# Optimization experiments

Hardware: AMD Instinct MI355X
Metric: run time of the kernel (lower is better)

## Reference

```python
import jax, jax.numpy as jnp
import numpy as np

H, B, F, D1, D21, D22, C = 10, 16384, 4, 2048, 2048, 2048, 2
OBS_X, OBS_Y, RADIUS = 40.0, 15.0, 6.0


def setup_inputs() -> dict:
    key = jax.random.key(0)
    ks = jax.random.split(key, 12)
    s = 0.02  # weight scale
    return {
        'x':   jax.random.normal(ks[0], (B, F), jnp.float32),
        'W1':  jax.random.normal(ks[1], (H, F, D1), jnp.float32) * s,
        'b1':  jnp.zeros((H, D1), jnp.float32),
        'W21': jax.random.normal(ks[2], (H, D1, D21), jnp.float32) * s,
        'b21': jnp.zeros((H, D21), jnp.float32),
        'W22': jax.random.normal(ks[3], (H, D1, D22), jnp.float32) * s,
        'b22': jnp.zeros((H, D22), jnp.float32),
        'W31': jax.random.normal(ks[4], (H, D21, C), jnp.float32) * s,
        'b31': jnp.zeros((H, C), jnp.float32),
        'W32': jax.random.normal(ks[5], (H, D22, C), jnp.float32) * s,
        'b32': jnp.zeros((H, C), jnp.float32),
        'wt':  jnp.ones((H,), jnp.float32),
        'mean': jax.random.normal(ks[6], (F,), jnp.float32),
        'std':  jnp.ones((F,), jnp.float32),
        'sgn': 1,
        'itr': 0,
    }


def reference(x, W1, b1, W21, b21, W22, b22, W31, b31, W32, b32, wt, mean, std, sgn, itr):
    # x: [B,F]; un-normalized state x0 = x*std + mean
    x0 = x * std + mean

    # --- 10-head small-MLP ensemble (batched over heads via einsum) ---
    h1  = jax.nn.relu(jnp.einsum('bf,hfd->hbd', x, W1) + b1[:, None, :])      # [H,B,D1]
    x21 = jax.nn.relu(jnp.einsum('hbd,hde->hbe', h1, W21) + b21[:, None, :])  # [H,B,D21]
    x22 = jax.nn.relu(jnp.einsum('hbd,hde->hbe', h1, W22) + b22[:, None, :])  # [H,B,D22]
    x31 = jnp.einsum('hbe,hec->hbc', x21, W31) + b31[:, None, :]              # [H,B,C] nominal control
    x32 = 4.0 * jax.nn.sigmoid(jnp.einsum('hbe,hec->hbc', x22, W32) + b32[:, None, :])  # [H,B,C] CBF params

    # --- dCBF constraint (shared across heads; depends only on x0) ---
    px, py, theta, v = x0[:, 0], x0[:, 1], x0[:, 2], x0[:, 3]
    dx, dy = px - OBS_X, py - OBS_Y
    st, ct = jnp.sin(theta), jnp.cos(theta)
    barrier = dx * dx + dy * dy - RADIUS * RADIUS                 # [B]
    barrier_dot = 2.0 * dx * v * ct + 2.0 * dy * v * st          # [B]
    Lf2b = 2.0 * v * v                                            # [B]
    LgLfbu1 = -2.0 * dx * v * st + 2.0 * dy * v * ct
    LgLfbu2 = 2.0 * dx * ct + 2.0 * dy * st
    G = jnp.stack([-LgLfbu1, -LgLfbu2], axis=-1)                  # [B,C]

    # sgn == 1 -> same branch for every head (i==0 or sgn==1)
    h_rhs = Lf2b + (x32[..., 0] + x32[..., 1]) * barrier_dot + x32[..., 0] * x32[..., 1] * barrier  # [H,B]

    # --- batched QP: min 0.5 u'u - x31'u  s.t. G u <= h  (Q = I) ---
    # closed-form single-constraint active set: u = x31 - relu(G.x31 - h)/||G||^2 * G
    Gu = jnp.einsum('bc,hbc->hb', G, x31)                         # [H,B]
    GG = jnp.sum(G * G, axis=-1)                                  # [B]
    lam = jax.nn.relu(Gu - h_rhs) / GG                            # [H,B]
    u = x31 - lam[..., None] * G[None, :, :]                      # [H,B,C]

    # --- softmax-weighted ensemble sum ---
    w = jax.nn.softmax(wt)                                        # [H]
    return jnp.einsum('h,hbc->bc', w, u)                          # [B,C]
```

## Files before the change

### kernel.cpp

```cpp
#include <hip/hip_runtime.h>
#include <hip/hip_bf16.h>
#include <stdint.h>

#define H_  10
#define B_  16384
#define F_  4
#define D_  2048
#define C_  2

typedef __attribute__((ext_vector_type(8)))  short  short8;
typedef __attribute__((ext_vector_type(16))) float  floatx16;

typedef const uint32_t __attribute__((address_space(1))) gu32;
typedef uint32_t       __attribute__((address_space(3))) lu32;

__device__ __forceinline__ void async16(const void* g, void* l) {
    __builtin_amdgcn_global_load_lds((gu32*)g, (lu32*)l, 16, 0, 0);
}

__device__ __forceinline__ short8 bc8(uint4 v) { return __builtin_bit_cast(short8, v); }

__device__ __forceinline__ uint32_t packbf(float a, float b) {
    a = fmaxf(a, 0.f); b = fmaxf(b, 0.f);
    const uint32_t ax = __builtin_bit_cast(uint32_t, a) + 0x8000u;
    const uint32_t bx = __builtin_bit_cast(uint32_t, b) + 0x8000u;
    return (ax >> 16) | (bx & 0xFFFF0000u);
}

__device__ __forceinline__ uint32_t f2bf(float f) {
    union { float f; uint32_t u; } a; a.f = f;
    uint32_t u = a.u;
    u += 0x7FFF + ((u >> 16) & 1);
    return u >> 16;
}
__device__ __forceinline__ uint32_t pack2bf(float a, float b) {
    return f2bf(a) | (f2bf(b) << 16);
}


__global__ __launch_bounds__(256) void k_convert(
    const float* __restrict__ W21, const float* __restrict__ W22,
    uint16_t* __restrict__ Bc)
{
    __shared__ float tile[64][65];
    const int z = blockIdx.z;
    const int h = z % H_;
    const float* src = (z < H_ ? W21 : W22) + (size_t)h * D_ * D_;
    uint16_t*   dst  = Bc + (size_t)h * 2 * D_ * D_ + (z < H_ ? 0 : (size_t)D_ * D_);
    const int k0 = blockIdx.x * 64, n0 = blockIdx.y * 64;
    const int t = threadIdx.x;

    const int c4 = (t & 15) * 4;
    const int rb = (t >> 4) * 4;
#pragma unroll
    for (int i = 0; i < 4; i++) {
        const float4 v = *(const float4*)(src + (size_t)(k0 + rb + i) * D_ + n0 + c4);
        tile[rb + i][c4 + 0] = v.x; tile[rb + i][c4 + 1] = v.y;
        tile[rb + i][c4 + 2] = v.z; tile[rb + i][c4 + 3] = v.w;
    }
    __syncthreads();
    const int n = t >> 2;
    const int cb = (t & 3) * 2;
#pragma unroll
    for (int j = 0; j < 2; j++) {
        const int kk = (cb + j) * 8;
        uint32_t pk[4];
#pragma unroll
        for (int e = 0; e < 4; e++)
            pk[e] = pack2bf(tile[kk + 2 * e][n], tile[kk + 2 * e + 1][n]);
        *(uint4*)(dst + (size_t)(n0 + n) * D_ + k0 + kk) = make_uint4(pk[0], pk[1], pk[2], pk[3]);
    }
}

__global__ __launch_bounds__(256) void k_zero(uint4* p, int n4) {
    const int i = blockIdx.x * 256 + threadIdx.x;
    if (i < n4) p[i] = make_uint4(0u, 0u, 0u, 0u);
}

__global__ __launch_bounds__(256) void k_h1(
    const float* __restrict__ x, const float* __restrict__ W1,
    const float* __restrict__ b1, uint16_t* __restrict__ h1t, int h)
{
    const int t = threadIdx.x;
    const int kc = t & 127;
    const int rh = t >> 7;
    const int k0 = kc * 16;
    const float* W1h = W1 + (size_t)h * F_ * D_;
    float w[4][16], bb[16];
#pragma unroll
    for (int f = 0; f < 4; f++)
#pragma unroll
        for (int j = 0; j < 16; j += 4) {
            const float4 v = *(const float4*)(W1h + f * D_ + k0 + j);
            w[f][j] = v.x; w[f][j+1] = v.y; w[f][j+2] = v.z; w[f][j+3] = v.w;
        }
#pragma unroll
    for (int j = 0; j < 16; j += 4) {
        const float4 v = *(const float4*)(b1 + (size_t)h * D_ + k0 + j);
        bb[j] = v.x; bb[j+1] = v.y; bb[j+2] = v.z; bb[j+3] = v.w;
    }
    const int rowBase = blockIdx.x * 16 + rh * 8;
#pragma unroll
    for (int rr = 0; rr < 8; rr++) {
        const int row = rowBase + rr;
        const float4 xv = *(const float4*)(x + (size_t)row * 4);
        uint32_t pk[8];
#pragma unroll
        for (int j = 0; j < 16; j += 2) {
            float aa = fmaf(xv.x, w[0][j], bb[j]);
            aa = fmaf(xv.y, w[1][j], aa);
            aa = fmaf(xv.z, w[2][j], aa);
            aa = fmaf(xv.w, w[3][j], aa);
            float bv = fmaf(xv.x, w[0][j+1], bb[j+1]);
            bv = fmaf(xv.y, w[1][j+1], bv);
            bv = fmaf(xv.z, w[2][j+1], bv);
            bv = fmaf(xv.w, w[3][j+1], bv);
            pk[j >> 1] = packbf(aa, bv);
        }
        uint16_t* d = h1t + (size_t)row * D_ + k0;
        *(uint4*)d       = make_uint4(pk[0], pk[1], pk[2], pk[3]);
        *(uint4*)(d + 8) = make_uint4(pk[4], pk[5], pk[6], pk[7]);
    }
}

__global__ __launch_bounds__(256, 2) void k_gemm(
    const uint16_t* __restrict__ h1t, const uint16_t* __restrict__ Bcw,
    const float* __restrict__ b21, const float* __restrict__ b22,
    const float* __restrict__ W31, const float* __restrict__ W32,
    float* __restrict__ acc31, float* __restrict__ acc32, int h)
{
    __shared__ uint4 smem[3072];

    const int bid = blockIdx.x;
    const int xcd = bid & 7, idx = bid >> 3;
    const int mt = xcd * 16 + (idx & 15), nt = idx >> 4;
    const int mBase = mt * 128, nBase = nt * 256;

    const int t = threadIdx.x;
    const int lane = t & 63, wid = t >> 6;
    const int l31 = lane & 31, hi = lane >> 5;

    const int srow   = lane >> 3;
    const int schunk = (lane & 7) ^ srow;

    const uint16_t* Ag = h1t + (size_t)(mBase + wid * 8 + srow) * D_ + schunk * 8;
    const uint16_t* Bg = Bcw + (size_t)h * (4096 * (size_t)D_)
                             + (size_t)(nBase + wid * 8 + srow) * D_ + schunk * 8;

    floatx16 acc[4][2];
#pragma unroll
    for (int mi = 0; mi < 4; mi++)
#pragma unroll
        for (int nj = 0; nj < 2; nj++)
#pragma unroll
            for (int e = 0; e < 16; e++) acc[mi][nj][e] = 0.f;

    const int x7 = l31 & 7;

    for (int kt = 0; kt < D_; kt += 64) {
#pragma unroll
        for (int i = 0; i < 4; i++)
            async16(Ag + (size_t)(i * 32) * D_ + kt, smem + i * 256 + wid * 64);
#pragma unroll
        for (int i = 0; i < 8; i++)
            async16(Bg + (size_t)(i * 32) * D_ + kt, smem + 1024 + i * 256 + wid * 64);
        asm volatile("s_waitcnt vmcnt(0)" ::: "memory");
        __builtin_amdgcn_sched_barrier(0);
        __builtin_amdgcn_s_barrier();

        __builtin_amdgcn_s_setprio(1);
#pragma unroll
        for (int kk = 0; kk < 4; kk++) {
            const int cx = (kk * 2 + hi) ^ x7;
            short8 af[4], bf[2];
#pragma unroll
            for (int mi = 0; mi < 4; mi++)
                af[mi] = bc8(smem[(mi * 32 + l31) * 8 + cx]);
#pragma unroll
            for (int nj = 0; nj < 2; nj++)
                bf[nj] = bc8(smem[1024 + (wid * 64 + nj * 32 + l31) * 8 + cx]);
#pragma unroll
            for (int mi = 0; mi < 4; mi++)
#pragma unroll
                for (int nj = 0; nj < 2; nj++)
                    acc[mi][nj] = __builtin_amdgcn_mfma_f32_32x32x16_bf16(
                        af[mi], bf[nj], acc[mi][nj], 0, 0, 0);
        }
        __builtin_amdgcn_s_setprio(0);
        __syncthreads();
    }

    const int p    = nBase >> 11;
    const int nloc = nBase & 2047;
    const float* b2p = (p ? b22 : b21) + (size_t)h * D_;
    const float* W3p = (p ? W32 : W31) + (size_t)h * D_ * C_;
    float* ab = (p ? acc32 : acc31) + (size_t)h * B_ * C_;

    float bs[2], w3x[2], w3y[2];
#pragma unroll
    for (int nj = 0; nj < 2; nj++) {
        const int e = nloc + wid * 64 + nj * 32 + l31;
        bs[nj] = b2p[e];
        const float2 w2 = *(const float2*)(W3p + e * 2);
        w3x[nj] = w2.x; w3y[nj] = w2.y;
    }
#pragma unroll
    for (int mi = 0; mi < 4; mi++)
#pragma unroll
        for (int r = 0; r < 16; r++) {
            const float v0 = fmaxf(acc[mi][0][r] + bs[0], 0.f);
            const float v1 = fmaxf(acc[mi][1][r] + bs[1], 0.f);
            float s0 = fmaf(v0, w3x[0], v1 * w3x[1]);
            float s1 = fmaf(v0, w3y[0], v1 * w3y[1]);
#pragma unroll
            for (int off = 1; off < 32; off <<= 1) {
                s0 += __shfl_xor(s0, off, 64);
                s1 += __shfl_xor(s1, off, 64);
            }
            if (l31 == 0) {
                const int row = mBase + mi * 32 + (r & 3) + 8 * (r >> 2) + 4 * hi;
                atomicAdd(&ab[row * C_ + 0], s0);
                atomicAdd(&ab[row * C_ + 1], s1);
            }
        }
}

__global__ __launch_bounds__(256) void k_final(
    const float* __restrict__ x,
    const float* __restrict__ acc31, const float* __restrict__ acc32,
    const float* __restrict__ b31, const float* __restrict__ b32,
    const float* __restrict__ wt, const float* __restrict__ mean,
    const float* __restrict__ stdv, float* __restrict__ out)
{
    const int b = blockIdx.x * 256 + threadIdx.x;
    const float4 xb = *(const float4*)(x + (size_t)b * 4);
    const float px = xb.x * stdv[0] + mean[0];
    const float py = xb.y * stdv[1] + mean[1];
    const float th = xb.z * stdv[2] + mean[2];
    const float v  = xb.w * stdv[3] + mean[3];
    const float dx = px - 40.0f, dy = py - 15.0f;
    const float st = sinf(th), ct = cosf(th);
    const float barrier = dx * dx + dy * dy - 36.0f;
    const float bdot = 2.f * dx * v * ct + 2.f * dy * v * st;
    const float Lf2b = 2.f * v * v;
    const float G0 = -(-2.f * dx * v * st + 2.f * dy * v * ct);
    const float G1 = -(2.f * dx * ct + 2.f * dy * st);
    const float GG = G0 * G0 + G1 * G1;

    float we[H_];
    float wmax = wt[0];
    for (int h = 1; h < H_; h++) wmax = fmaxf(wmax, wt[h]);
    float wsum = 0.f;
    for (int h = 0; h < H_; h++) { we[h] = expf(wt[h] - wmax); wsum += we[h]; }

    float o0 = 0.f, o1 = 0.f;
#pragma unroll
    for (int h = 0; h < H_; h++) {
        const size_t idx = ((size_t)h * B_ + b) * 2;
        const float x310 = acc31[idx]     + b31[h * 2];
        const float x311 = acc31[idx + 1] + b31[h * 2 + 1];
        const float z0 = acc32[idx]     + b32[h * 2];
        const float z1 = acc32[idx + 1] + b32[h * 2 + 1];
        const float x320 = 4.f / (1.f + expf(-z0));
        const float x321 = 4.f / (1.f + expf(-z1));
        const float hr = Lf2b + (x320 + x321) * bdot + x320 * x321 * barrier;
        const float Gu = G0 * x310 + G1 * x311;
        const float lam = fmaxf(Gu - hr, 0.f) / GG;
        o0 += we[h] * (x310 - lam * G0);
        o1 += we[h] * (x311 - lam * G1);
    }
    out[b * 2]     = o0 / wsum;
    out[b * 2 + 1] = o1 / wsum;
}

extern "C" void kernel_launch(void* const* d_in, const int* in_sizes, int n_in,
                              void* d_out, int out_size, void* d_ws, size_t ws_size,
                              hipStream_t stream)
{
    const float* x    = (const float*)d_in[0];
    const float* W1   = (const float*)d_in[1];
    const float* b1   = (const float*)d_in[2];
    const float* W21  = (const float*)d_in[3];
    const float* b21  = (const float*)d_in[4];
    const float* W22  = (const float*)d_in[5];
    const float* b22  = (const float*)d_in[6];
    const float* W31  = (const float*)d_in[7];
    const float* b31  = (const float*)d_in[8];
    const float* W32  = (const float*)d_in[9];
    const float* b32  = (const float*)d_in[10];
    const float* wt   = (const float*)d_in[11];
    const float* mean = (const float*)d_in[12];
    const float* stdv = (const float*)d_in[13];
    float* out = (float*)d_out;

    char* ws = (char*)d_ws;
    uint16_t* Bc   = (uint16_t*)(ws);
    float* acc31   = (float*)(ws + 167772160);
    float* acc32   = (float*)(ws + 169082880);
    uint16_t* h1t  = (uint16_t*)(ws + 170393600);

    k_convert<<<dim3(32, 32, 20), 256, 0, stream>>>(W21, W22, Bc);
    k_zero<<<dim3(640), 256, 0, stream>>>((uint4*)acc31, 163840);
    for (int h = 0; h < H_; ++h) {
        k_h1<<<dim3(1024), 256, 0, stream>>>(x, W1, b1, h1t, h);
        k_gemm<<<dim3(2048), 256, 0, stream>>>(h1t, Bc, b21, b22, W31, W32,
                                               acc31, acc32, h);
    }
    k_final<<<dim3(64), 256, 0, stream>>>(x, acc31, acc32, b31, b32, wt, mean, stdv, out);
}
```

Measured before the change: 3.342 ms.

## Software-pipeline GEMM main loop with double-buffered B and register-staged A

The GEMM K-loop now prefetches the next B tile into a second LDS buffer with async global-to-LDS loads, and loads A two steps ahead into registers, writing it to a single LDS slot between barriers. This overlaps global memory latency with the MFMA compute of the current tile, where before each iteration waited for its own loads. LDS use grows to 80 KB of dynamic shared memory, set through a function attribute, and A staging uses more registers. Both could lower occupancy under launch_bounds(256,2).

```diff
diff --git a/kernel.cpp b/kernel.cpp
--- a/kernel.cpp
+++ b/kernel.cpp
@@ -129,7 +129,7 @@
     const float* __restrict__ W31, const float* __restrict__ W32,
     float* __restrict__ acc31, float* __restrict__ acc32, int h)
 {
-    __shared__ uint4 smem[3072];
+    extern __shared__ uint4 smem[];
 
     const int bid = blockIdx.x;
     const int xcd = bid & 7, idx = bid >> 3;
@@ -147,6 +147,24 @@
     const uint16_t* Bg = Bcw + (size_t)h * (4096 * (size_t)D_)
                              + (size_t)(nBase + wid * 8 + srow) * D_ + schunk * 8;
 
+    uint4 pa[4];
+    auto loadA = [&](int kt) {
+#pragma unroll
+        for (int i = 0; i < 4; i++)
+            pa[i] = *(const uint4*)(Ag + (size_t)(i * 32) * D_ + kt);
+    };
+    auto writeA = [&]() {
+#pragma unroll
+        for (int i = 0; i < 4; i++)
+            smem[i * 256 + wid * 64 + lane] = pa[i];
+    };
+    auto stageB = [&](int buf, int kt) {
+#pragma unroll
+        for (int i = 0; i < 8; i++)
+            async16(Bg + (size_t)(i * 32) * D_ + kt,
+                    smem + 1024 + buf * 2048 + i * 256 + wid * 64);
+    };
+
     floatx16 acc[4][2];
 #pragma unroll
     for (int mi = 0; mi < 4; mi++)
@@ -157,16 +175,20 @@
 
     const int x7 = l31 & 7;
 
-    for (int kt = 0; kt < D_; kt += 64) {
-#pragma unroll
-        for (int i = 0; i < 4; i++)
-            async16(Ag + (size_t)(i * 32) * D_ + kt, smem + i * 256 + wid * 64);
-#pragma unroll
-        for (int i = 0; i < 8; i++)
-            async16(Bg + (size_t)(i * 32) * D_ + kt, smem + 1024 + i * 256 + wid * 64);
-        asm volatile("s_waitcnt vmcnt(0)" ::: "memory");
-        __builtin_amdgcn_sched_barrier(0);
-        __builtin_amdgcn_s_barrier();
+    stageB(0, 0);
+    loadA(0);
+    asm volatile("s_waitcnt vmcnt(0)" ::: "memory");
+    __builtin_amdgcn_sched_barrier(0);
+    writeA();
+    stageB(1, 64);
+    asm volatile("s_waitcnt lgkmcnt(0)" ::: "memory");
+    __builtin_amdgcn_sched_barrier(0);
+    loadA(64);
+    __builtin_amdgcn_s_barrier();
+    __builtin_amdgcn_sched_barrier(0);
+
+    for (int tt = 0; tt < 32; ++tt) {
+        const uint4* Bb = smem + 1024 + (tt & 1) * 2048;
 
         __builtin_amdgcn_s_setprio(1);
 #pragma unroll
@@ -178,7 +200,7 @@
                 af[mi] = bc8(smem[(mi * 32 + l31) * 8 + cx]);
 #pragma unroll
             for (int nj = 0; nj < 2; nj++)
-                bf[nj] = bc8(smem[1024 + (wid * 64 + nj * 32 + l31) * 8 + cx]);
+                bf[nj] = bc8(Bb[(wid * 64 + nj * 32 + l31) * 8 + cx]);
 #pragma unroll
             for (int mi = 0; mi < 4; mi++)
 #pragma unroll
@@ -187,7 +209,18 @@
                         af[mi], bf[nj], acc[mi][nj], 0, 0, 0);
         }
         __builtin_amdgcn_s_setprio(0);
-        __syncthreads();
+        if (tt == 31) break;
+
+        __builtin_amdgcn_s_barrier();
+        asm volatile("s_waitcnt vmcnt(0)" ::: "memory");
+        __builtin_amdgcn_sched_barrier(0);
+        writeA();
+        if (tt < 30) stageB(tt & 1, (tt + 2) * 64);
+        asm volatile("s_waitcnt lgkmcnt(0)" ::: "memory");
+        __builtin_amdgcn_sched_barrier(0);
+        if (tt < 30) loadA((tt + 2) * 64);
+        __builtin_amdgcn_s_barrier();
+        __builtin_amdgcn_sched_barrier(0);
     }
 
     const int p    = nBase >> 11;
@@ -299,12 +332,19 @@
     float* acc32   = (float*)(ws + 169082880);
     uint16_t* h1t  = (uint16_t*)(ws + 170393600);
 
+    static bool attr_done = false;
+    if (!attr_done) {
+        hipFuncSetAttribute(reinterpret_cast<const void*>(k_gemm),
+                            hipFuncAttributeMaxDynamicSharedMemorySize, 81920);
+        attr_done = true;
+    }
+
     k_convert<<<dim3(32, 32, 20), 256, 0, stream>>>(W21, W22, Bc);
     k_zero<<<dim3(640), 256, 0, stream>>>((uint4*)acc31, 163840);
     for (int h = 0; h < H_; ++h) {
         k_h1<<<dim3(1024), 256, 0, stream>>>(x, W1, b1, h1t, h);
-        k_gemm<<<dim3(2048), 256, 0, stream>>>(h1t, Bc, b21, b22, W31, W32,
-                                               acc31, acc32, h);
+        k_gemm<<<dim3(2048), 256, 81920, stream>>>(h1t, Bc, b21, b22, W31, W32,
+                                                   acc31, acc32, h);
     }
     k_final<<<dim3(64), 256, 0, stream>>>(x, acc31, acc32, b31, b32, wt, mean, stdv, out);
 }
```

Result: slower. 5.095 ms (+52.4%).

## Double-buffer GEMM K-tiles with async LDS loads to overlap memory and MFMA

Applied to the files above, without the earlier changes.

Replaces the single-buffered 64-wide K loop with a two-stage pipeline of 32-wide K tiles. Each tile is prefetched with global_load_lds while the previous one is consumed, and partial vmcnt waits keep one tile in flight. The LDS layout is remapped so two rows share each 128-byte line, with a new XOR swizzle. The aim is to hide global load latency behind MFMA work. The cost is twice as many barriers per unit of K and more complex addressing.

```diff
diff --git a/kernel.cpp b/kernel.cpp
--- a/kernel.cpp
+++ b/kernel.cpp
@@ -140,12 +140,35 @@
     const int lane = t & 63, wid = t >> 6;
     const int l31 = lane & 31, hi = lane >> 5;
 
-    const int srow   = lane >> 3;
-    const int schunk = (lane & 7) ^ srow;
-
-    const uint16_t* Ag = h1t + (size_t)(mBase + wid * 8 + srow) * D_ + schunk * 8;
-    const uint16_t* Bg = Bcw + (size_t)h * (4096 * (size_t)D_)
-                             + (size_t)(nBase + wid * 8 + srow) * D_ + schunk * 8;
+    const uint16_t* Abase = h1t + (size_t)mBase * D_;
+    const uint16_t* Bbase = Bcw + (size_t)h * (4096 * (size_t)D_) + (size_t)nBase * D_;
+    int aoff[2], boff[4];
+#pragma unroll
+    for (int j = 0; j < 2; j++) {
+        const int unit = j * 256 + t;
+        const int rp = unit >> 3, uu = (unit & 7) ^ (rp & 7);
+        aoff[j] = (rp * 2 + (uu & 1)) * D_ + (uu >> 1) * 8;
+    }
+#pragma unroll
+    for (int j = 0; j < 4; j++) {
+        const int unit = j * 256 + t;
+        const int rp = unit >> 3, uu = (unit & 7) ^ (rp & 7);
+        boff[j] = (rp * 2 + (uu & 1)) * D_ + (uu >> 1) * 8;
+    }
+    const int wbase = wid * 64;
+
+    auto stageTile = [&](int buf, int kt) {
+#pragma unroll
+        for (int j = 0; j < 2; j++)
+            async16(Abase + aoff[j] + kt, smem + buf * 512 + j * 256 + wbase);
+#pragma unroll
+        for (int j = 0; j < 4; j++)
+            async16(Bbase + boff[j] + kt, smem + 1024 + buf * 1024 + j * 256 + wbase);
+    };
+
+    const int rpl = l31 >> 1;
+    const int par = l31 & 1;
+    const int x7p = rpl & 7;
 
     floatx16 acc[4][2];
 #pragma unroll
@@ -155,30 +178,29 @@
 #pragma unroll
             for (int e = 0; e < 16; e++) acc[mi][nj][e] = 0.f;
 
-    const int x7 = l31 & 7;
-
-    for (int kt = 0; kt < D_; kt += 64) {
-#pragma unroll
-        for (int i = 0; i < 4; i++)
-            async16(Ag + (size_t)(i * 32) * D_ + kt, smem + i * 256 + wid * 64);
-#pragma unroll
-        for (int i = 0; i < 8; i++)
-            async16(Bg + (size_t)(i * 32) * D_ + kt, smem + 1024 + i * 256 + wid * 64);
-        asm volatile("s_waitcnt vmcnt(0)" ::: "memory");
+    stageTile(0, 0);
+    stageTile(1, 32);
+
+    for (int tt = 0; tt < 64; ++tt) {
+        if (tt == 63) { asm volatile("s_waitcnt vmcnt(0)" ::: "memory"); }
+        else          { asm volatile("s_waitcnt vmcnt(6)" ::: "memory"); }
         __builtin_amdgcn_sched_barrier(0);
         __builtin_amdgcn_s_barrier();
 
+        const int ab = (tt & 1) * 512;
+        const int bb = 1024 + (tt & 1) * 1024;
+
         __builtin_amdgcn_s_setprio(1);
 #pragma unroll
-        for (int kk = 0; kk < 4; kk++) {
-            const int cx = (kk * 2 + hi) ^ x7;
+        for (int kk = 0; kk < 2; kk++) {
+            const int u = ((((kk * 2 + hi) << 1) | par) ^ x7p);
             short8 af[4], bf[2];
 #pragma unroll
             for (int mi = 0; mi < 4; mi++)
-                af[mi] = bc8(smem[(mi * 32 + l31) * 8 + cx]);
+                af[mi] = bc8(smem[ab + (mi * 16 + rpl) * 8 + u]);
 #pragma unroll
             for (int nj = 0; nj < 2; nj++)
-                bf[nj] = bc8(smem[1024 + (wid * 64 + nj * 32 + l31) * 8 + cx]);
+                bf[nj] = bc8(smem[bb + (wid * 32 + nj * 16 + rpl) * 8 + u]);
 #pragma unroll
             for (int mi = 0; mi < 4; mi++)
 #pragma unroll
@@ -187,14 +209,17 @@
                         af[mi], bf[nj], acc[mi][nj], 0, 0, 0);
         }
         __builtin_amdgcn_s_setprio(0);
-        __syncthreads();
+
+        __builtin_amdgcn_s_barrier();
+        __builtin_amdgcn_sched_barrier(0);
+        if (tt < 62) stageTile(tt & 1, (tt + 2) * 32);
     }
 
     const int p    = nBase >> 11;
     const int nloc = nBase & 2047;
     const float* b2p = (p ? b22 : b21) + (size_t)h * D_;
     const float* W3p = (p ? W32 : W31) + (size_t)h * D_ * C_;
-    float* ab = (p ? acc32 : acc31) + (size_t)h * B_ * C_;
+    float* ab2 = (p ? acc32 : acc31) + (size_t)h * B_ * C_;
 
     float bs[2], w3x[2], w3y[2];
 #pragma unroll
@@ -219,8 +244,8 @@
             }
             if (l31 == 0) {
                 const int row = mBase + mi * 32 + (r & 3) + 8 * (r >> 2) + 4 * hi;
-                atomicAdd(&ab[row * C_ + 0], s0);
-                atomicAdd(&ab[row * C_ + 1], s1);
+                atomicAdd(&ab2[row * C_ + 0], s0);
+                atomicAdd(&ab2[row * C_ + 1], s1);
             }
         }
 }
```

Result: slower. 3.682 ms (+10.2%).

## Shrink GEMM block tile to 128x128 with 2x2 warp grid for higher occupancy

Applied to the files above, without the earlier changes.

The GEMM block tile shrinks from 128x256 to 128x128, arranged as a 2x2 grid of 64x64 warp tiles, and twice as many blocks are launched. LDS use drops to 32KB, the launch bound rises to 4 blocks per CU, and the LDS swizzle gains an extra XOR term. The goal is more resident waves to hide the unpipelined load-then-compute loop. In exchange, each block does less MFMA work per byte loaded, and the epilogue issues more atomics.

```diff
diff --git a/kernel.cpp b/kernel.cpp
--- a/kernel.cpp
+++ b/kernel.cpp
@@ -123,47 +123,53 @@
     }
 }
 
-__global__ __launch_bounds__(256, 2) void k_gemm(
+__global__ __launch_bounds__(256, 4) void k_gemm(
     const uint16_t* __restrict__ h1t, const uint16_t* __restrict__ Bcw,
     const float* __restrict__ b21, const float* __restrict__ b22,
     const float* __restrict__ W31, const float* __restrict__ W32,
     float* __restrict__ acc31, float* __restrict__ acc32, int h)
 {
-    __shared__ uint4 smem[3072];
+    __shared__ uint4 smem[2048];
 
     const int bid = blockIdx.x;
     const int xcd = bid & 7, idx = bid >> 3;
     const int mt = xcd * 16 + (idx & 15), nt = idx >> 4;
-    const int mBase = mt * 128, nBase = nt * 256;
+    const int mBase = mt * 128, nBase = nt * 128;
 
     const int t = threadIdx.x;
     const int lane = t & 63, wid = t >> 6;
     const int l31 = lane & 31, hi = lane >> 5;
-
-    const int srow   = lane >> 3;
-    const int schunk = (lane & 7) ^ srow;
-
-    const uint16_t* Ag = h1t + (size_t)(mBase + wid * 8 + srow) * D_ + schunk * 8;
-    const uint16_t* Bg = Bcw + (size_t)h * (4096 * (size_t)D_)
-                             + (size_t)(nBase + wid * 8 + srow) * D_ + schunk * 8;
-
-    floatx16 acc[4][2];
-#pragma unroll
-    for (int mi = 0; mi < 4; mi++)
+    const int wm = wid >> 1, wn = wid & 1;
+
+    const uint16_t* Abase = h1t + (size_t)mBase * D_;
+    const uint16_t* Bbase = Bcw + (size_t)h * (4096 * (size_t)D_) + (size_t)nBase * D_;
+    int soff[4];
+#pragma unroll
+    for (int j = 0; j < 4; j++) {
+        const int unit = j * 256 + t;
+        const int row = unit >> 3;
+        const int cc = (unit & 7) ^ (row & 7) ^ ((row >> 3) & 3);
+        soff[j] = row * D_ + cc * 8;
+    }
+    const int wbase = wid * 64;
+
+    floatx16 acc[2][2];
+#pragma unroll
+    for (int mi = 0; mi < 2; mi++)
 #pragma unroll
         for (int nj = 0; nj < 2; nj++)
 #pragma unroll
             for (int e = 0; e < 16; e++) acc[mi][nj][e] = 0.f;
 
-    const int x7 = l31 & 7;
+    const int x7 = l31 & 7, s3 = l31 >> 3;
 
     for (int kt = 0; kt < D_; kt += 64) {
 #pragma unroll
-        for (int i = 0; i < 4; i++)
-            async16(Ag + (size_t)(i * 32) * D_ + kt, smem + i * 256 + wid * 64);
-#pragma unroll
-        for (int i = 0; i < 8; i++)
-            async16(Bg + (size_t)(i * 32) * D_ + kt, smem + 1024 + i * 256 + wid * 64);
+        for (int j = 0; j < 4; j++)
+            async16(Abase + soff[j] + kt, smem + j * 256 + wbase);
+#pragma unroll
+        for (int j = 0; j < 4; j++)
+            async16(Bbase + soff[j] + kt, smem + 1024 + j * 256 + wbase);
         asm volatile("s_waitcnt vmcnt(0)" ::: "memory");
         __builtin_amdgcn_sched_barrier(0);
         __builtin_amdgcn_s_barrier();
@@ -171,16 +177,16 @@
         __builtin_amdgcn_s_setprio(1);
 #pragma unroll
         for (int kk = 0; kk < 4; kk++) {
-            const int cx = (kk * 2 + hi) ^ x7;
-            short8 af[4], bf[2];
-#pragma unroll
-            for (int mi = 0; mi < 4; mi++)
-                af[mi] = bc8(smem[(mi * 32 + l31) * 8 + cx]);
+            const int u7 = (kk * 2 + hi) ^ x7 ^ s3;
+            short8 af[2], bf[2];
+#pragma unroll
+            for (int mi = 0; mi < 2; mi++)
+                af[mi] = bc8(smem[(wm * 64 + mi * 32 + l31) * 8 + u7]);
 #pragma unroll
             for (int nj = 0; nj < 2; nj++)
-                bf[nj] = bc8(smem[1024 + (wid * 64 + nj * 32 + l31) * 8 + cx]);
-#pragma unroll
-            for (int mi = 0; mi < 4; mi++)
+                bf[nj] = bc8(smem[1024 + (wn * 64 + nj * 32 + l31) * 8 + u7]);
+#pragma unroll
+            for (int mi = 0; mi < 2; mi++)
 #pragma unroll
                 for (int nj = 0; nj < 2; nj++)
                     acc[mi][nj] = __builtin_amdgcn_mfma_f32_32x32x16_bf16(
@@ -194,18 +200,18 @@
     const int nloc = nBase & 2047;
     const float* b2p = (p ? b22 : b21) + (size_t)h * D_;
     const float* W3p = (p ? W32 : W31) + (size_t)h * D_ * C_;
-    float* ab = (p ? acc32 : acc31) + (size_t)h * B_ * C_;
+    float* ab2 = (p ? acc32 : acc31) + (size_t)h * B_ * C_;
 
     float bs[2], w3x[2], w3y[2];
 #pragma unroll
     for (int nj = 0; nj < 2; nj++) {
-        const int e = nloc + wid * 64 + nj * 32 + l31;
+        const int e = nloc + wn * 64 + nj * 32 + l31;
         bs[nj] = b2p[e];
         const float2 w2 = *(const float2*)(W3p + e * 2);
         w3x[nj] = w2.x; w3y[nj] = w2.y;
     }
 #pragma unroll
-    for (int mi = 0; mi < 4; mi++)
+    for (int mi = 0; mi < 2; mi++)
 #pragma unroll
         for (int r = 0; r < 16; r++) {
             const float v0 = fmaxf(acc[mi][0][r] + bs[0], 0.f);
@@ -218,9 +224,9 @@
                 s1 += __shfl_xor(s1, off, 64);
             }
             if (l31 == 0) {
-                const int row = mBase + mi * 32 + (r & 3) + 8 * (r >> 2) + 4 * hi;
-                atomicAdd(&ab[row * C_ + 0], s0);
-                atomicAdd(&ab[row * C_ + 1], s1);
+                const int row = mBase + wm * 64 + mi * 32 + (r & 3) + 8 * (r >> 2) + 4 * hi;
+                atomicAdd(&ab2[row * C_ + 0], s0);
+                atomicAdd(&ab2[row * C_ + 1], s1);
             }
         }
 }
@@ -303,7 +309,7 @@
     k_zero<<<dim3(640), 256, 0, stream>>>((uint4*)acc31, 163840);
     for (int h = 0; h < H_; ++h) {
         k_h1<<<dim3(1024), 256, 0, stream>>>(x, W1, b1, h1t, h);
-        k_gemm<<<dim3(2048), 256, 0, stream>>>(h1t, Bc, b21, b22, W31, W32,
+        k_gemm<<<dim3(4096), 256, 0, stream>>>(h1t, Bc, b21, b22, W31, W32,
                                                acc31, acc32, h);
     }
     k_final<<<dim3(64), 256, 0, stream>>>(x, acc31, acc32, b31, b32, wt, mean, stdv, out);
```

After: 3.631 ms. +8.6%, slower.
